# Kernel optimization log

Measured on AMD Instinct MI355X. Metric: run time of the kernel, lower is better.

The kernel has to match this reference:

```python
import jax, jax.numpy as jnp
import numpy as np

B = 65536   # batch (number of parallel envs)
HID = 64    # GRU hidden / FC width
ACT = 3     # action count


def setup_inputs() -> dict:
    key = jax.random.key(0)
    ks = iter(jax.random.split(key, 64))

    def rn(shape, s=0.1):
        return jax.random.normal(next(ks), shape, dtype=jnp.float32) * s

    inp = {
        "obs": jax.random.uniform(next(ks), (B, 7, 7, 3), dtype=jnp.float32, maxval=10.0),
        "memory": rn((B, 4 * HID), 1.0),
        "conv_w1": rn((16, 3, 2, 2)), "conv_b1": rn((16,)),
        "conv_w2": rn((32, 16, 2, 2)), "conv_b2": rn((32,)),
        "conv_w3": rn((64, 32, 2, 2)), "conv_b3": rn((64,)),
    }
    for g in ("g1", "g2"):
        for l in (0, 1):
            inp[f"{g}_wih{l}"] = rn((3 * HID, HID))
            inp[f"{g}_whh{l}"] = rn((3 * HID, HID))
            inp[f"{g}_bih{l}"] = rn((3 * HID,))
            inp[f"{g}_bhh{l}"] = rn((3 * HID,))
    inp.update({
        "actor_w1": rn((HID, HID)), "actor_b1": rn((HID,)),
        "actor_w2": rn((ACT, HID)), "actor_b2": rn((ACT,)),
        "critic_w1": rn((HID, HID)), "critic_b1": rn((HID,)),
        "critic_w2": rn((1, HID)), "critic_b2": rn((1,)),
    })
    return inp


def _conv(x, w, b):
    # NCHW, OIHW, VALID, stride 1 (matches nn.Conv2d defaults)
    y = jax.lax.conv_general_dilated(x, w, (1, 1), 'VALID',
                                     dimension_numbers=('NCHW', 'OIHW', 'NCHW'))
    return y + b[None, :, None, None]


def _maxpool2(x):
    return jax.lax.reduce_window(x, -jnp.inf, jax.lax.max,
                                 (1, 1, 2, 2), (1, 1, 2, 2), 'VALID')


def _gru_cell(x, h, wih, whh, bih, bhh):
    # PyTorch GRU cell math (gate order: r, z, n)
    gi = x @ wih.T + bih
    gh = h @ whh.T + bhh
    i_r, i_z, i_n = jnp.split(gi, 3, axis=-1)
    h_r, h_z, h_n = jnp.split(gh, 3, axis=-1)
    r = jax.nn.sigmoid(i_r + h_r)
    z = jax.nn.sigmoid(i_z + h_z)
    n = jnp.tanh(i_n + r * h_n)
    return (1.0 - z) * n + z * h


def reference(obs, memory, conv_w1, conv_b1, conv_w2, conv_b2, conv_w3, conv_b3,
              g1_wih0, g1_whh0, g1_bih0, g1_bhh0, g1_wih1, g1_whh1, g1_bih1, g1_bhh1,
              g2_wih0, g2_whh0, g2_bih0, g2_bhh0, g2_wih1, g2_whh1, g2_bih1, g2_bhh1,
              actor_w1, actor_b1, actor_w2, actor_b2,
              critic_w1, critic_b1, critic_w2, critic_b2):
    bsz = memory.shape[0]
    # obs.transpose(1,3).transpose(2,3): NHWC -> NCHW
    x = jnp.transpose(obs, (0, 3, 1, 2))
    x = jax.nn.relu(_conv(x, conv_w1, conv_b1))   # [B,16,6,6]
    x = _maxpool2(x)                              # [B,16,3,3]
    x = jax.nn.relu(_conv(x, conv_w2, conv_b2))   # [B,32,2,2]
    x = jax.nn.relu(_conv(x, conv_w3, conv_b3))   # [B,64,1,1]
    x = x.reshape(bsz, -1)                        # [B,64]

    h1 = memory[:, :2 * HID].reshape(bsz, 2, HID)
    h2 = memory[:, 2 * HID:].reshape(bsz, 2, HID)

    # single-timestep 2-layer GRU #1
    inp = x
    h1_new = []
    for l, (wih, whh, bih, bhh) in enumerate([(g1_wih0, g1_whh0, g1_bih0, g1_bhh0),
                                              (g1_wih1, g1_whh1, g1_bih1, g1_bhh1)]):
        inp = _gru_cell(inp, h1[:, l], wih, whh, bih, bhh)
        h1_new.append(inp)
    mem1 = jnp.stack(h1_new, axis=1).reshape(bsz, 2 * HID)

    # single-timestep 2-layer GRU #2 (input = GRU1 top-layer output)
    h2_new = []
    for l, (wih, whh, bih, bhh) in enumerate([(g2_wih0, g2_whh0, g2_bih0, g2_bhh0),
                                              (g2_wih1, g2_whh1, g2_bih1, g2_bhh1)]):
        inp = _gru_cell(inp, h2[:, l], wih, whh, bih, bhh)
        h2_new.append(inp)
    mem2 = jnp.stack(h2_new, axis=1).reshape(bsz, 2 * HID)

    embedding = inp  # GRU2 top-layer output, [B,64]

    logits = jax.nn.relu(embedding @ actor_w1.T + actor_b1) @ actor_w2.T + actor_b2
    log_probs = jax.nn.log_softmax(logits, axis=1)          # Categorical(logits=log_softmax)
    value = (jax.nn.relu(embedding @ critic_w1.T + critic_b1) @ critic_w2.T + critic_b2)[:, 0]
    memory_out = jnp.concatenate([mem1, mem2], axis=1)      # [B,256]
    return (log_probs, value, memory_out)
```

## Files before the change

### kernel.cpp

```cpp
#include <hip/hip_runtime.h>

#define BATCH 65536
#define NT 256
#define NTG 512
#define MFMA __builtin_amdgcn_mfma_f32_16x16x32_bf16

typedef short bf16x8 __attribute__((ext_vector_type(8)));
typedef float f32x4 __attribute__((ext_vector_type(4)));
typedef unsigned short u16x8 __attribute__((ext_vector_type(8)));
typedef unsigned short u16x4 __attribute__((ext_vector_type(4)));

__device__ __forceinline__ float sigmoidf_(float x) { return 1.0f / (1.0f + __expf(-x)); }
__device__ __forceinline__ float tanhf_(float x) { return 2.0f / (1.0f + __expf(-2.0f * x)) - 1.0f; }
__device__ __forceinline__ unsigned short f2b(float f) {
  union { float f; unsigned int u; } v; v.f = f;
  unsigned int r = (v.u + 0x7FFFu + ((v.u >> 16) & 1u)) >> 16;
  return (unsigned short)r;
}
__device__ __forceinline__ float b2f(unsigned short u) {
  return __uint_as_float(((unsigned int)u) << 16);
}
__device__ __forceinline__ bf16x8 cvt8(float4 a, float4 b) {
  union { unsigned short u[8]; bf16x8 v; } t;
  t.u[0] = f2b(a.x); t.u[1] = f2b(a.y); t.u[2] = f2b(a.z); t.u[3] = f2b(a.w);
  t.u[4] = f2b(b.x); t.u[5] = f2b(b.y); t.u[6] = f2b(b.z); t.u[7] = f2b(b.w);
  return t.v;
}

__global__ __launch_bounds__(NT) void k_prep(
    const float* __restrict__ W0, const float* __restrict__ W1,
    const float* __restrict__ W2, const float* __restrict__ W3,
    const float* __restrict__ W4, const float* __restrict__ W5,
    const float* __restrict__ W6, const float* __restrict__ W7,
    const float* __restrict__ bi0, const float* __restrict__ bi1,
    const float* __restrict__ bi2, const float* __restrict__ bi3,
    const float* __restrict__ bh0, const float* __restrict__ bh1,
    const float* __restrict__ bh2, const float* __restrict__ bh3,
    const float* __restrict__ aw1, const float* __restrict__ cw1,
    const float* __restrict__ w3s,
    unsigned short* __restrict__ wsW, unsigned short* __restrict__ wsH,
    unsigned short* __restrict__ wsW3, float* __restrict__ wsB) {
  const int y = blockIdx.y;
  const int i = blockIdx.x * NT + threadIdx.x;
  if (y < 8) {
    if (i >= 12288) return;
    const float* src = (y == 0) ? W0 : (y == 1) ? W1 : (y == 2) ? W2 : (y == 3) ? W3
                     : (y == 4) ? W4 : (y == 5) ? W5 : (y == 6) ? W6 : W7;
    const int c = y >> 1, p = y & 1;
    const int j = i >> 6, k = i & 63;
    const int g = j >> 6, jrow = j & 63;
    const int jt = jrow >> 4, r16i = jrow & 15;
    const int kseg = k >> 5, kgv = (k & 31) >> 3, e = k & 7;
    const int lane = kgv * 16 + r16i;
    const int q = g * 4 + p * 2 + kseg;
    wsW[c * 24576 + ((jt * 12 + q) * 64 + lane) * 8 + e] = f2b(src[i]);
  } else if (y == 8) {
    if (i < 4096) wsH[i] = f2b(aw1[i]);
  } else if (y == 9) {
    if (i < 4096) wsH[4096 + i] = f2b(cw1[i]);
  } else if (y == 10) {
    if (i < 8192) wsW3[i] = f2b(w3s[i]);
  } else {
    const int c = y - 11;
    if (i < 256) {
      const float* bi = (c == 0) ? bi0 : (c == 1) ? bi1 : (c == 2) ? bi2 : bi3;
      const float* bh = (c == 0) ? bh0 : (c == 1) ? bh1 : (c == 2) ? bh2 : bh3;
      const int j = i & 63, g = i >> 6;
      float v = (g == 0) ? bi[j] + bh[j]
              : (g == 1) ? bi[64 + j] + bh[64 + j]
              : (g == 2) ? bi[128 + j] : bh[128 + j];
      wsB[c * 256 + i] = v;
    }
  }
}

#define OSTR 149
#define PSTR 146
__global__ __launch_bounds__(NT) void k_conv12(const float* __restrict__ obs,
                                               const float* __restrict__ w1,
                                               const float* __restrict__ b1,
                                               const float* __restrict__ w2,
                                               const float* __restrict__ b2,
                                               unsigned short* __restrict__ c2b) {
  __shared__ float obs_f[64 * OSTR];
  __shared__ unsigned short pooled[64 * PSTR];
  const int tid = threadIdx.x;
  const int lane = tid & 63;
  const int wave = tid >> 6;
  const int m_base = blockIdx.x * 64;

  {
    const float4* src = (const float4*)(obs + (size_t)m_base * 147);
#pragma unroll 1
    for (int i = tid; i < 2352; i += NT) {
      const float4 v = src[i];
      int idx = i * 4;
      int s = idx / 147;
      int c = idx - s * 147;
      obs_f[s * OSTR + c] = v.x;
      if (++c == 147) { c = 0; ++s; } obs_f[s * OSTR + c] = v.y;
      if (++c == 147) { c = 0; ++s; } obs_f[s * OSTR + c] = v.z;
      if (++c == 147) { c = 0; ++s; } obs_f[s * OSTR + c] = v.w;
    }
  }
  __syncthreads();

  if (wave < 3) {
    const int ph = wave, s = lane;
    float r[3][21];
#pragma unroll
    for (int rr = 0; rr < 3; ++rr)
#pragma unroll
      for (int i = 0; i < 21; ++i) r[rr][i] = obs_f[s * OSTR + (2 * ph + rr) * 21 + i];
#pragma unroll 1
    for (int oc = 0; oc < 16; ++oc) {
      float wv[12];
#pragma unroll
      for (int i = 0; i < 12; ++i) wv[i] = w1[oc * 12 + i];
      const float bias = b1[oc];
#pragma unroll
      for (int pw = 0; pw < 3; ++pw) {
        float m = 0.0f;
#pragma unroll
        for (int dh = 0; dh < 2; ++dh)
#pragma unroll
          for (int dw = 0; dw < 2; ++dw) {
            float acc = bias;
#pragma unroll
            for (int kh = 0; kh < 2; ++kh)
#pragma unroll
              for (int kw = 0; kw < 2; ++kw)
#pragma unroll
                for (int c = 0; c < 3; ++c)
                  acc += r[dh + kh][(2 * pw + dw + kw) * 3 + c] * wv[c * 4 + kh * 2 + kw];
            m = fmaxf(m, fmaxf(acc, 0.0f));
          }
        pooled[s * PSTR + oc * 9 + ph * 3 + pw] = f2b(m);
      }
    }
  }
  __syncthreads();

  {
    const int g = wave, s = lane;
    const int ocb = g * 8;
    float acc[8][4];
#pragma unroll
    for (int u = 0; u < 8; ++u) {
      const float bb = b2[ocb + u];
      acc[u][0] = bb; acc[u][1] = bb; acc[u][2] = bb; acc[u][3] = bb;
    }
#pragma unroll 1
    for (int ic = 0; ic < 16; ++ic) {
      float p9[9];
#pragma unroll
      for (int p = 0; p < 9; ++p) p9[p] = b2f(pooled[s * PSTR + ic * 9 + p]);
#pragma unroll
      for (int u = 0; u < 8; ++u) {
        float w[4];
#pragma unroll
        for (int i = 0; i < 4; ++i) w[i] = w2[((ocb + u) * 16 + ic) * 4 + i];
#pragma unroll
        for (int oh = 0; oh < 2; ++oh)
#pragma unroll
          for (int ow = 0; ow < 2; ++ow)
            acc[u][oh * 2 + ow] += p9[(oh + 0) * 3 + (ow + 0)] * w[0] +
                                   p9[(oh + 0) * 3 + (ow + 1)] * w[1] +
                                   p9[(oh + 1) * 3 + (ow + 0)] * w[2] +
                                   p9[(oh + 1) * 3 + (ow + 1)] * w[3];
      }
    }
    unsigned short ob[32];
#pragma unroll
    for (int u = 0; u < 8; ++u)
#pragma unroll
      for (int p = 0; p < 4; ++p) ob[u * 4 + p] = f2b(fmaxf(acc[u][p], 0.0f));
#pragma unroll
    for (int i = 0; i < 4; ++i)
      *(u16x8*)(c2b + (size_t)(m_base + s) * 128 + g * 32 + 8 * i) = *(const u16x8*)(ob + 8 * i);
  }
}

#define XSTR 88
__global__ __launch_bounds__(NTG, 4) void k_gru(
    const unsigned short* __restrict__ c2b,
    const float* __restrict__ memF,
    const unsigned short* __restrict__ wsW,
    const unsigned short* __restrict__ wsW3,
    const float* __restrict__ wsB,
    const unsigned short* __restrict__ wsH,
    const float* __restrict__ b3,
    const float* __restrict__ ab1, const float* __restrict__ cb1,
    const float* __restrict__ aw2, const float* __restrict__ ab2,
    const float* __restrict__ cw2, const float* __restrict__ cb2,
    float* __restrict__ out) {
  __shared__ unsigned short wlds[24576];
  __shared__ unsigned short xls[128 * XSTR];
  const int tid = threadIdx.x;
  const int lane = tid & 63;
  const int wave = tid >> 6;
  const int r16 = lane & 15;
  const int kg = lane >> 4;
  const int wbase = wave * 16;
  const int m_base = blockIdx.x * 128 + wbase;
  float* outMem = out + (size_t)4 * BATCH;

  float4 wst[6];
  {
    const float4* wsrc = (const float4*)wsW;
#pragma unroll
    for (int r = 0; r < 6; ++r) wst[r] = wsrc[r * NTG + tid];
  }
  bf16x8 a0[4];
  {
    const unsigned short* ap = c2b + (size_t)(m_base + r16) * 128 + kg * 8;
#pragma unroll
    for (int f = 0; f < 4; ++f) a0[f] = *(const bf16x8*)(ap + f * 32);
  }
  float4 hraw[4];
  {
    const float* hp = memF + (size_t)(m_base + r16) * 256 + kg * 8;
    hraw[0] = *(const float4*)(hp);
    hraw[1] = *(const float4*)(hp + 4);
    hraw[2] = *(const float4*)(hp + 32);
    hraw[3] = *(const float4*)(hp + 36);
  }

#pragma unroll
  for (int n = 0; n < 4; ++n) {
    const unsigned short* bp = wsW3 + (size_t)(n * 16 + r16) * 128 + kg * 8;
    f32x4 q0 = (f32x4)(0.0f);
#pragma unroll
    for (int f = 0; f < 4; ++f) {
      bf16x8 b = *(const bf16x8*)(bp + f * 32);
      q0 = MFMA(b, a0[f], q0, 0, 0, 0);
    }
    const f32x4 b4 = *(const f32x4*)(b3 + n * 16 + kg * 4);
    u16x4 xo;
#pragma unroll
    for (int q = 0; q < 4; ++q) xo[q] = f2b(fmaxf(q0[q] + b4[q], 0.0f));
    *(u16x4*)(xls + (wbase + r16) * XSTR + n * 16 + kg * 4) = xo;
  }
  {
    float4* wd = (float4*)wlds;
#pragma unroll
    for (int r = 0; r < 6; ++r) wd[r * NTG + tid] = wst[r];
  }
  __syncthreads();

#pragma unroll 1
  for (int c = 0; c < 4; ++c) {
    const int co = c * 64;
    const float* bcp = wsB + c * 256;
    bf16x8 ax0, ax1, ah0, ah1;
    {
      const unsigned short* xp = xls + (wbase + r16) * XSTR + kg * 8;
      ax0 = *(const bf16x8*)(xp);
      ax1 = *(const bf16x8*)(xp + 32);
    }
    ah0 = cvt8(make_float4(hraw[0].x, hraw[0].y, hraw[0].z, hraw[0].w),
               make_float4(hraw[1].x, hraw[1].y, hraw[1].z, hraw[1].w));
    ah1 = cvt8(make_float4(hraw[2].x, hraw[2].y, hraw[2].z, hraw[2].w),
               make_float4(hraw[3].x, hraw[3].y, hraw[3].z, hraw[3].w));
    if (c < 3) {
      const float* hp = memF + (size_t)(m_base + r16) * 256 + (c + 1) * 64 + kg * 8;
      hraw[0] = *(const float4*)(hp);
      hraw[1] = *(const float4*)(hp + 4);
      hraw[2] = *(const float4*)(hp + 32);
      hraw[3] = *(const float4*)(hp + 36);
    }
    const unsigned short* wl = wlds + lane * 8;
#pragma unroll 1
    for (int jt = 0; jt < 4; ++jt) {
      const unsigned short* wjt = wl + jt * 6144;
      bf16x8 xr0 = *(const bf16x8*)(wjt);
      bf16x8 xr1 = *(const bf16x8*)(wjt + 512);
      bf16x8 hr0 = *(const bf16x8*)(wjt + 1024);
      bf16x8 hr1 = *(const bf16x8*)(wjt + 1536);
      bf16x8 xz0 = *(const bf16x8*)(wjt + 2048);
      bf16x8 xz1 = *(const bf16x8*)(wjt + 2560);
      bf16x8 hz0 = *(const bf16x8*)(wjt + 3072);
      bf16x8 hz1 = *(const bf16x8*)(wjt + 3584);
      bf16x8 xn0 = *(const bf16x8*)(wjt + 4096);
      bf16x8 xn1 = *(const bf16x8*)(wjt + 4608);
      bf16x8 hn0 = *(const bf16x8*)(wjt + 5120);
      bf16x8 hn1 = *(const bf16x8*)(wjt + 5632);
      f32x4 sr = (f32x4)(0.0f), sz = (f32x4)(0.0f), sn = (f32x4)(0.0f), tn = (f32x4)(0.0f);
      sr = MFMA(xr0, ax0, sr, 0, 0, 0);
      sr = MFMA(xr1, ax1, sr, 0, 0, 0);
      sr = MFMA(hr0, ah0, sr, 0, 0, 0);
      sr = MFMA(hr1, ah1, sr, 0, 0, 0);
      sz = MFMA(xz0, ax0, sz, 0, 0, 0);
      sz = MFMA(xz1, ax1, sz, 0, 0, 0);
      sz = MFMA(hz0, ah0, sz, 0, 0, 0);
      sz = MFMA(hz1, ah1, sz, 0, 0, 0);
      sn = MFMA(xn0, ax0, sn, 0, 0, 0);
      sn = MFMA(xn1, ax1, sn, 0, 0, 0);
      tn = MFMA(hn0, ah0, tn, 0, 0, 0);
      tn = MFMA(hn1, ah1, tn, 0, 0, 0);
      const int jb = jt * 16 + kg * 4;
      const f32x4 ho4 = *(const f32x4*)(memF + (size_t)(m_base + r16) * 256 + co + jb);
      const f32x4 rb4 = *(const f32x4*)(bcp + jb);
      const f32x4 zb4 = *(const f32x4*)(bcp + 64 + jb);
      const f32x4 ib4 = *(const f32x4*)(bcp + 128 + jb);
      const f32x4 hb4 = *(const f32x4*)(bcp + 192 + jb);
      f32x4 nhv;
      u16x4 xo;
#pragma unroll
      for (int q = 0; q < 4; ++q) {
        const float rg = sigmoidf_(sr[q] + rb4[q]);
        const float zg = sigmoidf_(sz[q] + zb4[q]);
        const float ng = tanhf_((sn[q] + ib4[q]) + rg * (tn[q] + hb4[q]));
        const float nh = (1.0f - zg) * ng + zg * ho4[q];
        nhv[q] = nh;
        xo[q] = f2b(nh);
      }
      *(f32x4*)(outMem + (size_t)(m_base + r16) * 256 + co + jb) = nhv;
      *(u16x4*)(xls + (wbase + r16) * XSTR + jb) = xo;
    }
    if (c < 3) {
      __syncthreads();
      const float4* wsrc = (const float4*)(wsW + (size_t)(c + 1) * 24576);
      float4* wd = (float4*)wlds;
#pragma unroll
      for (int r = 0; r < 6; ++r) wd[r * NTG + tid] = wsrc[r * NTG + tid];
      __syncthreads();
    }
  }

  bf16x8 ex0, ex1;
  {
    const unsigned short* xp = xls + (wbase + r16) * XSTR + kg * 8;
    ex0 = *(const bf16x8*)(xp);
    ex1 = *(const bf16x8*)(xp + 32);
  }
  f32x4 ha[8];
#pragma unroll
  for (int n = 0; n < 8; ++n) ha[n] = (f32x4)(0.0f);
#pragma unroll
  for (int n = 0; n < 8; ++n) {
    const unsigned short* wp = wsH + (size_t)(n * 16 + r16) * 64 + kg * 8;
    bf16x8 b0 = *(const bf16x8*)(wp);
    bf16x8 b1 = *(const bf16x8*)(wp + 32);
    ha[n] = MFMA(b0, ex0, ha[n], 0, 0, 0);
    ha[n] = MFMA(b1, ex1, ha[n], 0, 0, 0);
  }
  float l0 = 0.0f, l1 = 0.0f, l2 = 0.0f, vv = 0.0f;
  const int jb0 = kg * 4;
#pragma unroll
  for (int t = 0; t < 4; ++t) {
    const f32x4 ba4 = *(const f32x4*)(ab1 + t * 16 + jb0);
    const f32x4 w0 = *(const f32x4*)(aw2 + t * 16 + jb0);
    const f32x4 w1 = *(const f32x4*)(aw2 + 64 + t * 16 + jb0);
    const f32x4 w2v = *(const f32x4*)(aw2 + 128 + t * 16 + jb0);
    const f32x4 bc4 = *(const f32x4*)(cb1 + t * 16 + jb0);
    const f32x4 wc4 = *(const f32x4*)(cw2 + t * 16 + jb0);
#pragma unroll
    for (int q = 0; q < 4; ++q) {
      const float av = fmaxf(ha[t][q] + ba4[q], 0.0f);
      const float cv = fmaxf(ha[t + 4][q] + bc4[q], 0.0f);
      l0 += av * w0[q]; l1 += av * w1[q]; l2 += av * w2v[q];
      vv += cv * wc4[q];
    }
  }
  l0 += __shfl_xor(l0, 16); l0 += __shfl_xor(l0, 32);
  l1 += __shfl_xor(l1, 16); l1 += __shfl_xor(l1, 32);
  l2 += __shfl_xor(l2, 16); l2 += __shfl_xor(l2, 32);
  vv += __shfl_xor(vv, 16); vv += __shfl_xor(vv, 32);
  if (kg == 0) {
    const int sq = m_base + r16;
    const float g0 = l0 + ab2[0], g1 = l1 + ab2[1], g2 = l2 + ab2[2];
    const float mx = fmaxf(g0, fmaxf(g1, g2));
    const float lse = mx + __logf(__expf(g0 - mx) + __expf(g1 - mx) + __expf(g2 - mx));
    out[(size_t)sq * 3 + 0] = g0 - lse;
    out[(size_t)sq * 3 + 1] = g1 - lse;
    out[(size_t)sq * 3 + 2] = g2 - lse;
    out[(size_t)3 * BATCH + sq] = vv + cb2[0];
  }
}

extern "C" void kernel_launch(void* const* d_in, const int* in_sizes, int n_in,
                              void* d_out, int out_size, void* d_ws, size_t ws_size,
                              hipStream_t stream) {
  (void)in_sizes; (void)n_in; (void)out_size; (void)ws_size;
  const float* obs = (const float*)d_in[0];
  const float* mem = (const float*)d_in[1];
  const float* w1 = (const float*)d_in[2];
  const float* b1 = (const float*)d_in[3];
  const float* w2 = (const float*)d_in[4];
  const float* b2 = (const float*)d_in[5];
  const float* w3 = (const float*)d_in[6];
  const float* b3 = (const float*)d_in[7];
  const float* gw[16];
  for (int i = 0; i < 16; ++i) gw[i] = (const float*)d_in[8 + i];
  const float* aw1 = (const float*)d_in[24];
  const float* ab1 = (const float*)d_in[25];
  const float* aw2 = (const float*)d_in[26];
  const float* ab2 = (const float*)d_in[27];
  const float* cw1 = (const float*)d_in[28];
  const float* cb1 = (const float*)d_in[29];
  const float* cw2 = (const float*)d_in[30];
  const float* cb2 = (const float*)d_in[31];

  float* out = (float*)d_out;

  unsigned short* c2b = (unsigned short*)d_ws;
  unsigned short* wsW = c2b + (size_t)128 * BATCH;
  unsigned short* wsH = wsW + 98304;
  unsigned short* wsW3 = wsH + 8192;
  float* wsB = (float*)(wsW3 + 8192);

  const dim3 blk(NT);
  hipLaunchKernelGGL(k_prep, dim3(48, 15), blk, 0, stream,
                     gw[0], gw[1], gw[4], gw[5], gw[8], gw[9], gw[12], gw[13],
                     gw[2], gw[6], gw[10], gw[14],
                     gw[3], gw[7], gw[11], gw[15],
                     aw1, cw1, w3, wsW, wsH, wsW3, wsB);
  hipLaunchKernelGGL(k_conv12, dim3(BATCH / 64), blk, 0, stream,
                     obs, w1, b1, w2, b2, c2b);
  hipLaunchKernelGGL(k_gru, dim3(BATCH / 128), dim3(NTG), 0, stream,
                     c2b, mem, wsW, wsW3, wsB, wsH, b3,
                     ab1, cb1, aw2, ab2, cw2, cb2, out);
}
```

Measured before the change: 112.2 us.

## Merge weight-prep and conv front-end into one kernel with split sample chunks

Folds the weight/bias preparation kernel into the conv1/conv2 kernel as extra blocks, removing one kernel launch and letting the small prep work overlap with the conv work. The conv part now handles its 64 samples in two chunks of 32. This halves the shared-memory footprint per block, which can raise occupancy. All 256 threads now share the conv1 work (192 active) and the conv2 work (4 output channels each), instead of 3 waves and 8 channels per thread. The cost is extra synchronisation, a serial loop over chunks, and some idle threads in the conv1 stage.

```diff
diff --git a/kernel.cpp b/kernel.cpp
--- a/kernel.cpp
+++ b/kernel.cpp
@@ -27,7 +27,12 @@
   return t.v;
 }
 
-__global__ __launch_bounds__(NT) void k_prep(
+#define OSTR 149
+#define PSTR 146
+__global__ __launch_bounds__(NT) void k_front(
+    const float* __restrict__ obs, const float* __restrict__ w1,
+    const float* __restrict__ b1, const float* __restrict__ w2,
+    const float* __restrict__ b2, unsigned short* __restrict__ c2b,
     const float* __restrict__ W0, const float* __restrict__ W1,
     const float* __restrict__ W2, const float* __restrict__ W3,
     const float* __restrict__ W4, const float* __restrict__ W5,
@@ -40,144 +45,146 @@
     const float* __restrict__ w3s,
     unsigned short* __restrict__ wsW, unsigned short* __restrict__ wsH,
     unsigned short* __restrict__ wsW3, float* __restrict__ wsB) {
-  const int y = blockIdx.y;
-  const int i = blockIdx.x * NT + threadIdx.x;
-  if (y < 8) {
-    if (i >= 12288) return;
-    const float* src = (y == 0) ? W0 : (y == 1) ? W1 : (y == 2) ? W2 : (y == 3) ? W3
-                     : (y == 4) ? W4 : (y == 5) ? W5 : (y == 6) ? W6 : W7;
-    const int c = y >> 1, p = y & 1;
-    const int j = i >> 6, k = i & 63;
-    const int g = j >> 6, jrow = j & 63;
-    const int jt = jrow >> 4, r16i = jrow & 15;
-    const int kseg = k >> 5, kgv = (k & 31) >> 3, e = k & 7;
-    const int lane = kgv * 16 + r16i;
-    const int q = g * 4 + p * 2 + kseg;
-    wsW[c * 24576 + ((jt * 12 + q) * 64 + lane) * 8 + e] = f2b(src[i]);
-  } else if (y == 8) {
-    if (i < 4096) wsH[i] = f2b(aw1[i]);
-  } else if (y == 9) {
-    if (i < 4096) wsH[4096 + i] = f2b(cw1[i]);
-  } else if (y == 10) {
-    if (i < 8192) wsW3[i] = f2b(w3s[i]);
-  } else {
-    const int c = y - 11;
-    if (i < 256) {
-      const float* bi = (c == 0) ? bi0 : (c == 1) ? bi1 : (c == 2) ? bi2 : bi3;
-      const float* bh = (c == 0) ? bh0 : (c == 1) ? bh1 : (c == 2) ? bh2 : bh3;
-      const int j = i & 63, g = i >> 6;
-      float v = (g == 0) ? bi[j] + bh[j]
-              : (g == 1) ? bi[64 + j] + bh[64 + j]
-              : (g == 2) ? bi[128 + j] : bh[128 + j];
-      wsB[c * 256 + i] = v;
-    }
-  }
-}
-
-#define OSTR 149
-#define PSTR 146
-__global__ __launch_bounds__(NT) void k_conv12(const float* __restrict__ obs,
-                                               const float* __restrict__ w1,
-                                               const float* __restrict__ b1,
-                                               const float* __restrict__ w2,
-                                               const float* __restrict__ b2,
-                                               unsigned short* __restrict__ c2b) {
-  __shared__ float obs_f[64 * OSTR];
-  __shared__ unsigned short pooled[64 * PSTR];
   const int tid = threadIdx.x;
-  const int lane = tid & 63;
-  const int wave = tid >> 6;
-  const int m_base = blockIdx.x * 64;
-
-  {
-    const float4* src = (const float4*)(obs + (size_t)m_base * 147);
-#pragma unroll 1
-    for (int i = tid; i < 2352; i += NT) {
-      const float4 v = src[i];
-      int idx = i * 4;
-      int s = idx / 147;
-      int c = idx - s * 147;
-      obs_f[s * OSTR + c] = v.x;
-      if (++c == 147) { c = 0; ++s; } obs_f[s * OSTR + c] = v.y;
-      if (++c == 147) { c = 0; ++s; } obs_f[s * OSTR + c] = v.z;
-      if (++c == 147) { c = 0; ++s; } obs_f[s * OSTR + c] = v.w;
-    }
-  }
-  __syncthreads();
-
-  if (wave < 3) {
-    const int ph = wave, s = lane;
-    float r[3][21];
-#pragma unroll
-    for (int rr = 0; rr < 3; ++rr)
-#pragma unroll
-      for (int i = 0; i < 21; ++i) r[rr][i] = obs_f[s * OSTR + (2 * ph + rr) * 21 + i];
-#pragma unroll 1
-    for (int oc = 0; oc < 16; ++oc) {
-      float wv[12];
-#pragma unroll
-      for (int i = 0; i < 12; ++i) wv[i] = w1[oc * 12 + i];
-      const float bias = b1[oc];
-#pragma unroll
-      for (int pw = 0; pw < 3; ++pw) {
-        float m = 0.0f;
-#pragma unroll
-        for (int dh = 0; dh < 2; ++dh)
-#pragma unroll
-          for (int dw = 0; dw < 2; ++dw) {
-            float acc = bias;
-#pragma unroll
-            for (int kh = 0; kh < 2; ++kh)
-#pragma unroll
-              for (int kw = 0; kw < 2; ++kw)
-#pragma unroll
-                for (int c = 0; c < 3; ++c)
-                  acc += r[dh + kh][(2 * pw + dw + kw) * 3 + c] * wv[c * 4 + kh * 2 + kw];
-            m = fmaxf(m, fmaxf(acc, 0.0f));
-          }
-        pooled[s * PSTR + oc * 9 + ph * 3 + pw] = f2b(m);
-      }
-    }
-  }
-  __syncthreads();
-
-  {
-    const int g = wave, s = lane;
-    const int ocb = g * 8;
-    float acc[8][4];
-#pragma unroll
-    for (int u = 0; u < 8; ++u) {
-      const float bb = b2[ocb + u];
-      acc[u][0] = bb; acc[u][1] = bb; acc[u][2] = bb; acc[u][3] = bb;
-    }
-#pragma unroll 1
-    for (int ic = 0; ic < 16; ++ic) {
-      float p9[9];
-#pragma unroll
-      for (int p = 0; p < 9; ++p) p9[p] = b2f(pooled[s * PSTR + ic * 9 + p]);
-#pragma unroll
+  const int b = blockIdx.x;
+  __shared__ float obs_f[32 * OSTR];
+  __shared__ unsigned short pooled[32 * PSTR];
+
+  if (b >= 1024) {
+    const int pb = b - 1024;
+    const int y = pb / 48;
+    const int i = (pb % 48) * NT + tid;
+    if (y < 8) {
+      if (i >= 12288) return;
+      const float* src = (y == 0) ? W0 : (y == 1) ? W1 : (y == 2) ? W2 : (y == 3) ? W3
+                       : (y == 4) ? W4 : (y == 5) ? W5 : (y == 6) ? W6 : W7;
+      const int c = y >> 1, p = y & 1;
+      const int j = i >> 6, k = i & 63;
+      const int g = j >> 6, jrow = j & 63;
+      const int jt = jrow >> 4, r16i = jrow & 15;
+      const int kseg = k >> 5, kgv = (k & 31) >> 3, e = k & 7;
+      const int lane = kgv * 16 + r16i;
+      const int q = g * 4 + p * 2 + kseg;
+      wsW[c * 24576 + ((jt * 12 + q) * 64 + lane) * 8 + e] = f2b(src[i]);
+    } else if (y == 8) {
+      if (i < 4096) wsH[i] = f2b(aw1[i]);
+    } else if (y == 9) {
+      if (i < 4096) wsH[4096 + i] = f2b(cw1[i]);
+    } else if (y == 10) {
+      if (i < 8192) wsW3[i] = f2b(w3s[i]);
+    } else {
+      const int c = y - 11;
+      if (i < 256) {
+        const float* bi = (c == 0) ? bi0 : (c == 1) ? bi1 : (c == 2) ? bi2 : bi3;
+        const float* bh = (c == 0) ? bh0 : (c == 1) ? bh1 : (c == 2) ? bh2 : bh3;
+        const int j = i & 63, g = i >> 6;
+        float v = (g == 0) ? bi[j] + bh[j]
+                : (g == 1) ? bi[64 + j] + bh[64 + j]
+                : (g == 2) ? bi[128 + j] : bh[128 + j];
+        wsB[c * 256 + i] = v;
+      }
+    }
+    return;
+  }
+
+  const int m_base = b * 64;
+#pragma unroll 1
+  for (int cc = 0; cc < 2; ++cc) {
+    const int sbase = m_base + cc * 32;
+    {
+      const float4* src = (const float4*)(obs + (size_t)sbase * 147);
+#pragma unroll 1
+      for (int i = tid; i < 1176; i += NT) {
+        const float4 v = src[i];
+        int idx = i * 4;
+        int s = idx / 147;
+        int c = idx - s * 147;
+        obs_f[s * OSTR + c] = v.x;
+        if (++c == 147) { c = 0; ++s; } obs_f[s * OSTR + c] = v.y;
+        if (++c == 147) { c = 0; ++s; } obs_f[s * OSTR + c] = v.z;
+        if (++c == 147) { c = 0; ++s; } obs_f[s * OSTR + c] = v.w;
+      }
+    }
+    __syncthreads();
+    if (tid < 192) {
+      const int s = tid & 31;
+      const int r = tid >> 5;
+      const int ph = r % 3;
+      const int ocb = (r / 3) * 8;
+      float rw[3][21];
+#pragma unroll
+      for (int rr = 0; rr < 3; ++rr)
+#pragma unroll
+        for (int i = 0; i < 21; ++i) rw[rr][i] = obs_f[s * OSTR + (2 * ph + rr) * 21 + i];
+#pragma unroll 1
       for (int u = 0; u < 8; ++u) {
-        float w[4];
-#pragma unroll
-        for (int i = 0; i < 4; ++i) w[i] = w2[((ocb + u) * 16 + ic) * 4 + i];
-#pragma unroll
-        for (int oh = 0; oh < 2; ++oh)
-#pragma unroll
-          for (int ow = 0; ow < 2; ++ow)
-            acc[u][oh * 2 + ow] += p9[(oh + 0) * 3 + (ow + 0)] * w[0] +
-                                   p9[(oh + 0) * 3 + (ow + 1)] * w[1] +
-                                   p9[(oh + 1) * 3 + (ow + 0)] * w[2] +
-                                   p9[(oh + 1) * 3 + (ow + 1)] * w[3];
-      }
-    }
-    unsigned short ob[32];
-#pragma unroll
-    for (int u = 0; u < 8; ++u)
-#pragma unroll
-      for (int p = 0; p < 4; ++p) ob[u * 4 + p] = f2b(fmaxf(acc[u][p], 0.0f));
-#pragma unroll
-    for (int i = 0; i < 4; ++i)
-      *(u16x8*)(c2b + (size_t)(m_base + s) * 128 + g * 32 + 8 * i) = *(const u16x8*)(ob + 8 * i);
+        const int oc = ocb + u;
+        float wv[12];
+#pragma unroll
+        for (int i = 0; i < 12; ++i) wv[i] = w1[oc * 12 + i];
+        const float bias = b1[oc];
+#pragma unroll
+        for (int pw = 0; pw < 3; ++pw) {
+          float m = 0.0f;
+#pragma unroll
+          for (int dh = 0; dh < 2; ++dh)
+#pragma unroll
+            for (int dw = 0; dw < 2; ++dw) {
+              float acc = bias;
+#pragma unroll
+              for (int kh = 0; kh < 2; ++kh)
+#pragma unroll
+                for (int kw = 0; kw < 2; ++kw)
+#pragma unroll
+                  for (int c = 0; c < 3; ++c)
+                    acc += rw[dh + kh][(2 * pw + dw + kw) * 3 + c] * wv[c * 4 + kh * 2 + kw];
+              m = fmaxf(m, fmaxf(acc, 0.0f));
+            }
+          pooled[s * PSTR + oc * 9 + ph * 3 + pw] = f2b(m);
+        }
+      }
+    }
+    __syncthreads();
+    {
+      const int s = tid & 31;
+      const int g = tid >> 5;
+      const int ocb = g * 4;
+      float acc[4][4];
+#pragma unroll
+      for (int u = 0; u < 4; ++u) {
+        const float bb = b2[ocb + u];
+        acc[u][0] = bb; acc[u][1] = bb; acc[u][2] = bb; acc[u][3] = bb;
+      }
+#pragma unroll 1
+      for (int ic = 0; ic < 16; ++ic) {
+        float p9[9];
+#pragma unroll
+        for (int p = 0; p < 9; ++p) p9[p] = b2f(pooled[s * PSTR + ic * 9 + p]);
+#pragma unroll
+        for (int u = 0; u < 4; ++u) {
+          float w[4];
+#pragma unroll
+          for (int i = 0; i < 4; ++i) w[i] = w2[((ocb + u) * 16 + ic) * 4 + i];
+#pragma unroll
+          for (int oh = 0; oh < 2; ++oh)
+#pragma unroll
+            for (int ow = 0; ow < 2; ++ow)
+              acc[u][oh * 2 + ow] += p9[(oh + 0) * 3 + (ow + 0)] * w[0] +
+                                     p9[(oh + 0) * 3 + (ow + 1)] * w[1] +
+                                     p9[(oh + 1) * 3 + (ow + 0)] * w[2] +
+                                     p9[(oh + 1) * 3 + (ow + 1)] * w[3];
+        }
+      }
+      unsigned short ob[16];
+#pragma unroll
+      for (int u = 0; u < 4; ++u)
+#pragma unroll
+        for (int p = 0; p < 4; ++p) ob[u * 4 + p] = f2b(fmaxf(acc[u][p], 0.0f));
+      unsigned short* dst = c2b + (size_t)(sbase + s) * 128 + ocb * 4;
+      *(u16x8*)(dst) = *(const u16x8*)(ob);
+      *(u16x8*)(dst + 8) = *(const u16x8*)(ob + 8);
+    }
+    __syncthreads();
   }
 }
 
@@ -232,8 +239,8 @@
     f32x4 q0 = (f32x4)(0.0f);
 #pragma unroll
     for (int f = 0; f < 4; ++f) {
-      bf16x8 b = *(const bf16x8*)(bp + f * 32);
-      q0 = MFMA(b, a0[f], q0, 0, 0, 0);
+      bf16x8 bb = *(const bf16x8*)(bp + f * 32);
+      q0 = MFMA(bb, a0[f], q0, 0, 0, 0);
     }
     const f32x4 b4 = *(const f32x4*)(b3 + n * 16 + kg * 4);
     u16x4 xo;
@@ -351,7 +358,7 @@
   for (int t = 0; t < 4; ++t) {
     const f32x4 ba4 = *(const f32x4*)(ab1 + t * 16 + jb0);
     const f32x4 w0 = *(const f32x4*)(aw2 + t * 16 + jb0);
-    const f32x4 w1 = *(const f32x4*)(aw2 + 64 + t * 16 + jb0);
+    const f32x4 w1v = *(const f32x4*)(aw2 + 64 + t * 16 + jb0);
     const f32x4 w2v = *(const f32x4*)(aw2 + 128 + t * 16 + jb0);
     const f32x4 bc4 = *(const f32x4*)(cb1 + t * 16 + jb0);
     const f32x4 wc4 = *(const f32x4*)(cw2 + t * 16 + jb0);
@@ -359,7 +366,7 @@
     for (int q = 0; q < 4; ++q) {
       const float av = fmaxf(ha[t][q] + ba4[q], 0.0f);
       const float cv = fmaxf(ha[t + 4][q] + bc4[q], 0.0f);
-      l0 += av * w0[q]; l1 += av * w1[q]; l2 += av * w2v[q];
+      l0 += av * w0[q]; l1 += av * w1v[q]; l2 += av * w2v[q];
       vv += cv * wc4[q];
     }
   }
@@ -410,14 +417,12 @@
   unsigned short* wsW3 = wsH + 8192;
   float* wsB = (float*)(wsW3 + 8192);
 
-  const dim3 blk(NT);
-  hipLaunchKernelGGL(k_prep, dim3(48, 15), blk, 0, stream,
+  hipLaunchKernelGGL(k_front, dim3(1024 + 720), dim3(NT), 0, stream,
+                     obs, w1, b1, w2, b2, c2b,
                      gw[0], gw[1], gw[4], gw[5], gw[8], gw[9], gw[12], gw[13],
                      gw[2], gw[6], gw[10], gw[14],
                      gw[3], gw[7], gw[11], gw[15],
                      aw1, cw1, w3, wsW, wsH, wsW3, wsB);
-  hipLaunchKernelGGL(k_conv12, dim3(BATCH / 64), blk, 0, stream,
-                     obs, w1, b1, w2, b2, c2b);
   hipLaunchKernelGGL(k_gru, dim3(BATCH / 128), dim3(NTG), 0, stream,
                      c2b, mem, wsW, wsW3, wsB, wsH, b3,
                      ab1, cb1, aw2, ab2, cw2, cb2, out);
```

Result: slower. 116.9 us (+4.2%).
